# Performance work log

Measured on AMD Instinct MI355X. Metric: run time of the kernel, lower is better.

The kernel has to match this reference:

```python
import jax, jax.numpy as jnp
import numpy as np

B, S, D, H = 1, 3072, 2048, 16
HD = D // H          # head_dim = 128
C = HD // 2          # rotary complex pairs = 64
EPS = 1e-6
WINDOW = 3           # frames of sliding-window attention on each side
L_TOKENS = 256       # tokens per frame (forward arg L)
NUM_FRAMES = S // L_TOKENS


def setup_inputs() -> dict:
    key = jax.random.key(0)
    ks = jax.random.split(key, 5)
    scale = 1.0 / np.sqrt(D)
    x = jax.random.normal(ks[0], (B, S, D), jnp.float32)
    wq = jax.random.normal(ks[1], (D, D), jnp.float32) * scale
    wk = jax.random.normal(ks[2], (D, D), jnp.float32) * scale
    wv = jax.random.normal(ks[3], (D, D), jnp.float32) * scale
    wo = jax.random.normal(ks[4], (D, D), jnp.float32) * scale
    bq = jnp.zeros((D,), jnp.float32)
    bk = jnp.zeros((D,), jnp.float32)
    bv = jnp.zeros((D,), jnp.float32)
    bo = jnp.zeros((D,), jnp.float32)
    gq = jnp.ones((D,), jnp.float32)
    gk = jnp.ones((D,), jnp.float32)
    # rotary freqs as cos/sin of angle t * theta_c (source uses a complex [S,1,C] tensor)
    t = jnp.arange(S, dtype=jnp.float32)
    inv_freq = 1.0 / (10000.0 ** (jnp.arange(C, dtype=jnp.float32) / C))
    ang = t[:, None] * inv_freq[None, :]        # [S, C]
    cos = jnp.cos(ang)[:, None, :]              # [S, 1, C]
    sin = jnp.sin(ang)[:, None, :]              # [S, 1, C]
    return {"x": x, "wq": wq, "bq": bq, "wk": wk, "bk": bk, "wv": wv,
            "bv": bv, "wo": wo, "bo": bo, "gq": gq, "gk": gk,
            "cos": cos, "sin": sin, "f": NUM_FRAMES, "L": L_TOKENS}


def _rms_norm(h, g, eps=EPS):
    # tensor_parallel_rms_norm with tp_size=1: fp32 variance, rsqrt, scale by weight
    hf = h.astype(jnp.float32)
    var = jnp.mean(hf * hf, axis=-1, keepdims=True)
    return (hf * jax.lax.rsqrt(var + eps) * g).astype(h.dtype)


def _rope(h, cos, sin):
    # complex rotation on interleaved (real, imag) pairs per head (rope_apply_for3d)
    b, s, d = h.shape
    hd = 2 * cos.shape[-1]
    n = d // hd
    hr = h.reshape(b, s, n, hd)
    xr, xi = hr[..., 0::2], hr[..., 1::2]       # [b,s,n,C]
    c, sn = cos[None], sin[None]                # [1,s,1,C] broadcast over heads
    yr = xr * c - xi * sn
    yi = xr * sn + xi * c
    y = jnp.stack([yr, yi], axis=-1).reshape(b, s, n, hd)
    return y.reshape(b, s, d)


def reference(x, wq, bq, wk, bk, wv, bv, wo, bo, gq, gk, cos, sin, f, L):
    q = _rope(_rms_norm(x @ wq.T + bq, gq), cos, sin)
    k = _rope(_rms_norm(x @ wk.T + bk, gk), cos, sin)
    v = x @ wv.T + bv
    b, s, d = q.shape
    hd = 2 * cos.shape[-1]
    n = d // hd
    qh = q.reshape(b, s, n, hd)
    kh = k.reshape(b, s, n, hd)
    vh = v.reshape(b, s, n, hd)
    scale = 1.0 / np.sqrt(hd)
    scores = jnp.einsum('bqnd,bknd->bnqk', qh, kh) * scale
    win = L * WINDOW
    idx = jnp.arange(s)
    delta = idx[None, :] - idx[:, None]
    mask = (delta <= win) & (delta >= -win)
    scores = jnp.where(mask[None, None], scores, -jnp.inf)
    probs = jax.nn.softmax(scores, axis=-1)
    out = jnp.einsum('bnqk,bknd->bqnd', probs, vh).reshape(b, s, d)
    return out @ wo.T + bo
```

## Files before the change

kernel.cpp:

```cpp
#include <hip/hip_runtime.h>
#include <stdint.h>

typedef unsigned short u16;
typedef __attribute__((ext_vector_type(8))) short short8;
typedef __attribute__((ext_vector_type(4))) float f32x4;

#define S_LEN 3072
#define D_DIM 2048
#define WIN 768
#define INV_SQRT_HD 0.08838834764831845f
#define M_SHIFT 12.0f

__device__ __forceinline__ u16 f2bf(float x) {
  union { float f; uint32_t u; } v; v.f = x;
  uint32_t r = v.u + 0x7FFFu + ((v.u >> 16) & 1u);
  return (u16)(r >> 16);
}
__device__ __forceinline__ float bf2f(u16 x) {
  union { uint32_t u; float f; } v; v.u = ((uint32_t)x) << 16;
  return v.f;
}

__device__ __forceinline__ void load_lds16(const void* g, void* l) {
  __builtin_amdgcn_global_load_lds(
      (const __attribute__((address_space(1))) void*)g,
      (__attribute__((address_space(3))) void*)l, 16, 0, 0);
}

#define MFMA16(a, b, c) __builtin_amdgcn_mfma_f32_16x16x32_bf16((a), (b), (c), 0, 0, 0)

__global__ __launch_bounds__(256) void k_cvt(const float* __restrict__ in,
                                             u16* __restrict__ out, int n4) {
  int i = blockIdx.x * 256 + threadIdx.x;
  if (i >= n4) return;
  float4 v = ((const float4*)in)[i];
  ushort4 o;
  o.x = f2bf(v.x); o.y = f2bf(v.y); o.z = f2bf(v.z); o.w = f2bf(v.w);
  ((ushort4*)out)[i] = o;
}

__global__ __launch_bounds__(256) void k_cvt_w(const float* __restrict__ w0, const float* __restrict__ w1,
                                               const float* __restrict__ w2, const float* __restrict__ w3,
                                               u16* __restrict__ o0, u16* __restrict__ o1,
                                               u16* __restrict__ o2, u16* __restrict__ o3, int n4each) {
  int i = blockIdx.x * 256 + threadIdx.x;
  int seg = i / n4each, off = i - seg * n4each;
  const float* in = seg == 0 ? w0 : seg == 1 ? w1 : seg == 2 ? w2 : w3;
  u16* out = seg == 0 ? o0 : seg == 1 ? o1 : seg == 2 ? o2 : o3;
  float4 v = ((const float4*)in)[off];
  ushort4 o;
  o.x = f2bf(v.x); o.y = f2bf(v.y); o.z = f2bf(v.z); o.w = f2bf(v.w);
  ((ushort4*)out)[off] = o;
}

__device__ __forceinline__ void gemm_body(const u16* __restrict__ A, const u16* __restrict__ B,
                                          int m0, int n0, int t, f32x4 (*acc)[4],
                                          u16* lA, u16* lB) {
  const int lane = t & 63, w = t >> 6, lo = lane & 15, g = lane >> 4;
  const int wr = w >> 1, wc = w & 1;
  const int srow = t >> 2;
  const int sch = (t & 3) ^ ((srow ^ (srow >> 3)) & 3);
  const u16* ga = A + (size_t)(m0 + srow) * D_DIM + sch * 8;
  const u16* gb = B + (size_t)(n0 + srow) * D_DIM + sch * 8;
  for (int k0 = 0; k0 < D_DIM; k0 += 32) {
    load_lds16(ga + k0, &lA[t * 8]);
    load_lds16(ga + (size_t)64 * D_DIM + k0, &lA[2048 + t * 8]);
    load_lds16(gb + k0, &lB[t * 8]);
    load_lds16(gb + (size_t)64 * D_DIM + k0, &lB[2048 + t * 8]);
    __syncthreads();
    short8 af[4], bfr[4];
#pragma unroll
    for (int m = 0; m < 4; ++m) {
      const int R = wr * 64 + m * 16 + lo;
      af[m] = *(const short8*)&lA[R * 32 + ((g ^ ((R ^ (R >> 3)) & 3)) << 3)];
    }
#pragma unroll
    for (int n = 0; n < 4; ++n) {
      const int R = wc * 64 + n * 16 + lo;
      bfr[n] = *(const short8*)&lB[R * 32 + ((g ^ ((R ^ (R >> 3)) & 3)) << 3)];
    }
#pragma unroll
    for (int m = 0; m < 4; ++m)
#pragma unroll
      for (int n = 0; n < 4; ++n) acc[m][n] = MFMA16(af[m], bfr[n], acc[m][n]);
    __syncthreads();
  }
}

__global__ __launch_bounds__(256) void k_gemm_qkv(const u16* __restrict__ A,
                                                  const u16* __restrict__ Bq, const u16* __restrict__ Bk,
                                                  const u16* __restrict__ Bv,
                                                  const float* __restrict__ bq, const float* __restrict__ bk,
                                                  const float* __restrict__ bv,
                                                  u16* __restrict__ Qb, u16* __restrict__ Kb,
                                                  u16* __restrict__ Vb) {
  __shared__ u16 lA[128 * 32];
  __shared__ u16 lB[128 * 32];
  const int id = blockIdx.x;
  const int xcd = id & 7, local = id >> 3;
  const int m_idx = xcd * 3 + local / 48;
  const int n_idx = local % 48;
  const int m0 = m_idx * 128;
  const int seg = n_idx >> 4, n0 = (n_idx & 15) * 128;
  const u16* B = seg == 0 ? Bq : seg == 1 ? Bk : Bv;
  const float* bias = seg == 0 ? bq : seg == 1 ? bk : bv;
  u16* D = seg == 0 ? Qb : seg == 1 ? Kb : Vb;
  const int t = threadIdx.x;
  const int lane = t & 63, w = t >> 6, lo = lane & 15, g = lane >> 4;
  const int wr = w >> 1, wc = w & 1;
  const f32x4 zero4 = {0.f, 0.f, 0.f, 0.f};
  f32x4 acc[4][4];
#pragma unroll
  for (int m = 0; m < 4; ++m)
#pragma unroll
    for (int n = 0; n < 4; ++n) acc[m][n] = zero4;
  gemm_body(A, B, m0, n0, t, acc, lA, lB);
#pragma unroll
  for (int m = 0; m < 4; ++m) {
    const int row = m0 + wr * 64 + m * 16 + 4 * g;
#pragma unroll
    for (int n = 0; n < 4; ++n) {
      const int col = n0 + wc * 64 + n * 16 + lo;
      const float bb = bias[col];
#pragma unroll
      for (int r = 0; r < 4; ++r)
        D[(size_t)(row + r) * 2048 + col] = f2bf(acc[m][n][r] + bb);
    }
  }
}

__global__ __launch_bounds__(256) void k_gemm_wo(const u16* __restrict__ A,
                                                 const u16* __restrict__ B,
                                                 const float* __restrict__ bias,
                                                 float* __restrict__ C) {
  __shared__ u16 lA[128 * 32];
  __shared__ u16 lB[128 * 32];
  const int id = blockIdx.x;
  const int xcd = id & 7, local = id >> 3;
  const int m_idx = xcd * 3 + local / 16;
  const int n_idx = local % 16;
  const int m0 = m_idx * 128, n0 = n_idx * 128;
  const int t = threadIdx.x;
  const int lane = t & 63, w = t >> 6, lo = lane & 15, g = lane >> 4;
  const int wr = w >> 1, wc = w & 1;
  const f32x4 zero4 = {0.f, 0.f, 0.f, 0.f};
  f32x4 acc[4][4];
#pragma unroll
  for (int m = 0; m < 4; ++m)
#pragma unroll
    for (int n = 0; n < 4; ++n) acc[m][n] = zero4;
  gemm_body(A, B, m0, n0, t, acc, lA, lB);
#pragma unroll
  for (int m = 0; m < 4; ++m) {
    const int row = m0 + wr * 64 + m * 16 + 4 * g;
#pragma unroll
    for (int n = 0; n < 4; ++n) {
      const int col = n0 + wc * 64 + n * 16 + lo;
      const float bb = bias[col];
#pragma unroll
      for (int r = 0; r < 4; ++r)
        C[(size_t)(row + r) * 2048 + col] = acc[m][n][r] + bb;
    }
  }
}

__global__ __launch_bounds__(256) void k_rms_rope_b(const u16* __restrict__ H,
                                                    const float* __restrict__ gain,
                                                    const float* __restrict__ cosT,
                                                    const float* __restrict__ sinT,
                                                    u16* __restrict__ out) {
  const int s = blockIdx.x, t = threadIdx.x;
  const short8 hv = *(const short8*)(H + (size_t)s * D_DIM + t * 8);
  float h[8];
#pragma unroll
  for (int j = 0; j < 8; ++j) h[j] = bf2f((u16)hv[j]);
  float ss = 0.f;
#pragma unroll
  for (int j = 0; j < 8; ++j) ss += h[j] * h[j];
#pragma unroll
  for (int off = 32; off > 0; off >>= 1) ss += __shfl_xor(ss, off);
  __shared__ float red[4];
  if ((t & 63) == 0) red[t >> 6] = ss;
  __syncthreads();
  ss = red[0] + red[1] + red[2] + red[3];
  const float rs = rsqrtf(ss * (1.f / D_DIM) + 1e-6f);
  const float4 g0 = *(const float4*)(gain + t * 8);
  const float4 g1 = *(const float4*)(gain + t * 8 + 4);
  float y[8];
  y[0] = h[0] * rs * g0.x; y[1] = h[1] * rs * g0.y;
  y[2] = h[2] * rs * g0.z; y[3] = h[3] * rs * g0.w;
  y[4] = h[4] * rs * g1.x; y[5] = h[5] * rs * g1.y;
  y[6] = h[6] * rs * g1.z; y[7] = h[7] * rs * g1.w;
  const int cbase = ((t * 8) & 127) >> 1;
  short8 o8;
#pragma unroll
  for (int i = 0; i < 4; ++i) {
    const float cs = cosT[s * 64 + cbase + i];
    const float sn = sinT[s * 64 + cbase + i];
    const float yr = y[2 * i] * cs - y[2 * i + 1] * sn;
    const float yi = y[2 * i] * sn + y[2 * i + 1] * cs;
    o8[2 * i] = (short)f2bf(yr);
    o8[2 * i + 1] = (short)f2bf(yi);
  }
  *(short8*)(out + (size_t)s * D_DIM + t * 8) = o8;
}

__global__ __launch_bounds__(256) void k_transpose(const u16* __restrict__ in,
                                                   u16* __restrict__ out) {
  __shared__ u16 tile[64][72];
  const int s0 = blockIdx.x * 64, d0 = blockIdx.y * 64;
  const int t = threadIdx.x;
  const int r = t >> 3, c8 = (t & 7) * 8;
#pragma unroll
  for (int p = 0; p < 2; ++p) {
    short8 v = *(const short8*)&in[(size_t)(s0 + r + p * 32) * D_DIM + d0 + c8];
#pragma unroll
    for (int j = 0; j < 8; ++j) tile[r + p * 32][c8 + j] = (u16)v[j];
  }
  __syncthreads();
#pragma unroll
  for (int p = 0; p < 2; ++p) {
    const int dr = r + p * 32;
    short8 o;
#pragma unroll
    for (int j = 0; j < 8; ++j) o[j] = (short)tile[c8 + j][dr];
    *(short8*)&out[(size_t)(d0 + dr) * S_LEN + s0 + c8] = o;
  }
}

__global__ __launch_bounds__(256, 3) void k_attn5(const u16* __restrict__ Q,
                                                  const u16* __restrict__ Kmat,
                                                  const u16* __restrict__ Vt,
                                                  u16* __restrict__ Oa,
                                                  u16* __restrict__ Ob,
                                                  float* __restrict__ lbuf) {
  const int qt = blockIdx.x, h = blockIdx.y, z = blockIdx.z;
  const int t = threadIdx.x, w = t >> 6, lane = t & 63, lo = lane & 15, g = lane >> 4;
  const int q0 = qt * 128;
  const int wrow = q0 + w * 32;
  const size_t hoff = (size_t)h * 128;

  __shared__ u16 lK[2][32 * 128];
  __shared__ u16 lV[2][128 * 32];
  __shared__ u16 ldsp[4][32][40];

  short8 qf[2][4];
#pragma unroll
  for (int m = 0; m < 2; ++m) {
    const u16* qp = Q + (size_t)(wrow + m * 16 + lo) * D_DIM + hoff + g * 8;
#pragma unroll
    for (int c = 0; c < 4; ++c) qf[m][c] = *(const short8*)(qp + c * 32);
  }

  const f32x4 zero4 = {0.f, 0.f, 0.f, 0.f};
  f32x4 oacc[2][8];
#pragma unroll
  for (int m = 0; m < 2; ++m)
#pragma unroll
    for (int ct = 0; ct < 8; ++ct) oacc[m][ct] = zero4;
  float lrun[2][4] = {{0.f, 0.f, 0.f, 0.f}, {0.f, 0.f, 0.f, 0.f}};

  int jlo = q0 - WIN; if (jlo < 0) jlo = 0;
  int jhi = q0 + 127 + WIN + 1; if (jhi > S_LEN) jhi = S_LEN;
  const int NT = (jhi - jlo) >> 5;
  const int it0 = z * (NT >> 1), it1 = it0 + (NT >> 1);

  const int krow = t >> 4,          kch  = (t & 15) ^ (krow & 7);
  const int krow1 = (t + 256) >> 4, kch1 = (t & 15) ^ (krow1 & 7);
  const int vrow = t >> 2,          vch  = (t & 3) ^ ((vrow >> 1) & 3);
  const int vrow1 = (t + 256) >> 2, vch1 = (t & 3) ^ ((vrow1 >> 1) & 3);

#define STAGE5(buf, jj)                                                                              \
  do {                                                                                               \
    load_lds16(Kmat + (size_t)((jj) + krow) * D_DIM + hoff + (kch << 3), &lK[buf][t * 8]);           \
    load_lds16(Kmat + (size_t)((jj) + krow1) * D_DIM + hoff + (kch1 << 3), &lK[buf][(t + 256) * 8]); \
    load_lds16(Vt + (size_t)(hoff + vrow) * S_LEN + (jj) + (vch << 3), &lV[buf][t * 8]);             \
    load_lds16(Vt + (size_t)(hoff + vrow1) * S_LEN + (jj) + (vch1 << 3), &lV[buf][(t + 256) * 8]);   \
  } while (0)

  STAGE5(0, jlo + (it0 << 5));
  __syncthreads();
  int cur = 0;
  for (int it = it0; it < it1; ++it) {
    const int j0 = jlo + (it << 5);
    if (it + 1 < it1) STAGE5(cur ^ 1, j0 + 32);

    f32x4 sc[2][2];
    sc[0][0] = zero4; sc[0][1] = zero4; sc[1][0] = zero4; sc[1][1] = zero4;
#pragma unroll
    for (int half = 0; half < 2; ++half) {
#pragma unroll
      for (int c = 0; c < 4; ++c) {
        const short8 kf = *(const short8*)
            &lK[cur][(half * 16 + lo) * 128 + (((g + 4 * c) ^ (lo & 7)) << 3)];
        sc[0][half] = MFMA16(qf[0][c], kf, sc[0][half]);
        sc[1][half] = MFMA16(qf[1][c], kf, sc[1][half]);
      }
    }

    const int dq = j0 - q0;
    const bool interior = (dq >= -640) && (dq <= 736);
#pragma unroll
    for (int m = 0; m < 2; ++m) {
#pragma unroll
      for (int r = 0; r < 4; ++r) {
        float a0 = fmaf(sc[m][0][r], INV_SQRT_HD, -M_SHIFT);
        float a1 = fmaf(sc[m][1][r], INV_SQRT_HD, -M_SHIFT);
        if (!interior) {
          const int dk = j0 + lo - (wrow + m * 16 + 4 * g + r);
          if (dk < -WIN || dk > WIN) a0 = -3e38f;
          if (dk + 16 < -WIN || dk + 16 > WIN) a1 = -3e38f;
        }
        const float p0 = __expf(a0);
        const float p1 = __expf(a1);
        lrun[m][r] += p0 + p1;
        ldsp[w][m * 16 + 4 * g + r][lo] = f2bf(p0);
        ldsp[w][m * 16 + 4 * g + r][16 + lo] = f2bf(p1);
      }
    }

    const short8 pf0 = *(const short8*)&ldsp[w][lo][g * 8];
    const short8 pf1 = *(const short8*)&ldsp[w][16 + lo][g * 8];
#pragma unroll
    for (int ct = 0; ct < 8; ++ct) {
      const short8 vf = *(const short8*)
          &lV[cur][(ct * 16 + lo) * 32 + ((g ^ ((lo >> 1) & 3)) << 3)];
      oacc[0][ct] = MFMA16(pf0, vf, oacc[0][ct]);
      oacc[1][ct] = MFMA16(pf1, vf, oacc[1][ct]);
    }
    __syncthreads();
    cur ^= 1;
  }
#undef STAGE5

#pragma unroll
  for (int off = 8; off > 0; off >>= 1)
#pragma unroll
    for (int m = 0; m < 2; ++m)
#pragma unroll
      for (int r = 0; r < 4; ++r) lrun[m][r] += __shfl_xor(lrun[m][r], off);

  u16* Op = z ? Ob : Oa;
#pragma unroll
  for (int m = 0; m < 2; ++m)
#pragma unroll
    for (int r = 0; r < 4; ++r) {
      const int row = wrow + m * 16 + 4 * g + r;
#pragma unroll
      for (int ct = 0; ct < 8; ++ct)
        Op[(size_t)row * D_DIM + hoff + ct * 16 + lo] = f2bf(oacc[m][ct][r]);
      if (lo == 0) lbuf[(size_t)z * S_LEN * 16 + (size_t)row * 16 + h] = lrun[m][r];
    }
}

__global__ __launch_bounds__(256) void k_combine(const u16* __restrict__ Oa,
                                                 const u16* __restrict__ Ob,
                                                 const float* __restrict__ lbuf,
                                                 u16* __restrict__ out) {
  const int i = blockIdx.x * 256 + threadIdx.x;
  const int s = i >> 8, d8 = (i & 255) * 8, h = d8 >> 7;
  const float la = lbuf[(size_t)s * 16 + h];
  const float lb = lbuf[(size_t)S_LEN * 16 + (size_t)s * 16 + h];
  const float inv = 1.f / (la + lb);
  const size_t base = (size_t)s * D_DIM + d8;
  const short8 a = *(const short8*)(Oa + base);
  const short8 b = *(const short8*)(Ob + base);
  short8 o;
#pragma unroll
  for (int j = 0; j < 8; ++j)
    o[j] = (short)f2bf((bf2f((u16)a[j]) + bf2f((u16)b[j])) * inv);
  *(short8*)(out + base) = o;
}

extern "C" void kernel_launch(void* const* d_in, const int* in_sizes, int n_in,
                              void* d_out, int out_size, void* d_ws, size_t ws_size,
                              hipStream_t stream) {
  const float* x    = (const float*)d_in[0];
  const float* wq   = (const float*)d_in[1];
  const float* bq   = (const float*)d_in[2];
  const float* wk   = (const float*)d_in[3];
  const float* bk   = (const float*)d_in[4];
  const float* wv   = (const float*)d_in[5];
  const float* bv   = (const float*)d_in[6];
  const float* wo   = (const float*)d_in[7];
  const float* bo   = (const float*)d_in[8];
  const float* gq   = (const float*)d_in[9];
  const float* gk   = (const float*)d_in[10];
  const float* cosT = (const float*)d_in[11];
  const float* sinT = (const float*)d_in[12];

  char* ws = (char*)d_ws;
  const size_t WB = (size_t)D_DIM * D_DIM * 2;
  const size_t XB = (size_t)S_LEN * D_DIM * 2;
  u16*   wq_bf = (u16*)(ws);
  u16*   wk_bf = (u16*)(ws + WB);
  u16*   wv_bf = (u16*)(ws + 2 * WB);
  u16*   wo_bf = (u16*)(ws + 3 * WB);
  u16*   x_bf  = (u16*)(ws + 4 * WB);
  u16*   Q0b   = (u16*)(ws + 4 * WB + XB);
  u16*   K0b   = (u16*)(ws + 4 * WB + 2 * XB);
  u16*   V0b   = (u16*)(ws + 4 * WB + 3 * XB);
  float* lbuf  = (float*)(ws + 4 * WB + 4 * XB);
  u16* q_bf = x_bf;
  u16* k_bf = wq_bf;
  u16* vT   = Q0b;
  u16* Ob   = K0b;
  u16* Oa   = (u16*)d_out;
  u16* attn = V0b;

  const int nw4 = (D_DIM * D_DIM) / 4;
  const int nx4 = (S_LEN * D_DIM) / 4;
  k_cvt<<<nx4 / 256, 256, 0, stream>>>(x, x_bf, nx4);
  k_cvt_w<<<4 * nw4 / 256, 256, 0, stream>>>(wq, wk, wv, wo, wq_bf, wk_bf, wv_bf, wo_bf, nw4);

  k_gemm_qkv<<<1152, 256, 0, stream>>>(x_bf, wq_bf, wk_bf, wv_bf, bq, bk, bv, Q0b, K0b, V0b);

  k_rms_rope_b<<<S_LEN, 256, 0, stream>>>(Q0b, gq, cosT, sinT, q_bf);
  k_rms_rope_b<<<S_LEN, 256, 0, stream>>>(K0b, gk, cosT, sinT, k_bf);
  k_transpose<<<dim3(S_LEN / 64, D_DIM / 64), 256, 0, stream>>>(V0b, vT);

  k_attn5<<<dim3(S_LEN / 128, 16, 2), 256, 0, stream>>>(q_bf, k_bf, vT, Oa, Ob, lbuf);
  k_combine<<<(S_LEN * D_DIM / 8) / 256, 256, 0, stream>>>(Oa, Ob, lbuf, attn);

  k_gemm_wo<<<384, 256, 0, stream>>>(attn, wo_bf, bo, (float*)d_out);
}
```

Before: 262.9 us.

## Deepen GEMM K-tile, fuse V transpose into QKV epilogue, merge small kernels

The GEMM main loop now stages 64-wide K slices instead of 32, with an 8-way XOR swizzle. This halves the number of barrier-separated iterations at the cost of twice the LDS per block. The QKV GEMM writes V directly in transposed layout with 4-element vector stores, removing the separate transpose kernel and its extra read/write pass. The x/weight conversion kernels are merged into one launch, and the Q and K RMSNorm+RoPE kernels are merged into one grid, reducing launch count. Workspace aliasing is adjusted so that attn reuses the Q0b buffer.

```diff
diff --git a/kernel.cpp b/kernel.cpp
--- a/kernel.cpp
+++ b/kernel.cpp
@@ -29,60 +29,73 @@
 
 #define MFMA16(a, b, c) __builtin_amdgcn_mfma_f32_16x16x32_bf16((a), (b), (c), 0, 0, 0)
 
-__global__ __launch_bounds__(256) void k_cvt(const float* __restrict__ in,
-                                             u16* __restrict__ out, int n4) {
+__global__ __launch_bounds__(256) void k_cvt_all(const float* __restrict__ x,
+                                                 const float* __restrict__ w0, const float* __restrict__ w1,
+                                                 const float* __restrict__ w2, const float* __restrict__ w3,
+                                                 u16* __restrict__ xo,
+                                                 u16* __restrict__ o0, u16* __restrict__ o1,
+                                                 u16* __restrict__ o2, u16* __restrict__ o3,
+                                                 int n4x, int n4w) {
   int i = blockIdx.x * 256 + threadIdx.x;
-  if (i >= n4) return;
-  float4 v = ((const float4*)in)[i];
-  ushort4 o;
-  o.x = f2bf(v.x); o.y = f2bf(v.y); o.z = f2bf(v.z); o.w = f2bf(v.w);
-  ((ushort4*)out)[i] = o;
-}
-
-__global__ __launch_bounds__(256) void k_cvt_w(const float* __restrict__ w0, const float* __restrict__ w1,
-                                               const float* __restrict__ w2, const float* __restrict__ w3,
-                                               u16* __restrict__ o0, u16* __restrict__ o1,
-                                               u16* __restrict__ o2, u16* __restrict__ o3, int n4each) {
-  int i = blockIdx.x * 256 + threadIdx.x;
-  int seg = i / n4each, off = i - seg * n4each;
-  const float* in = seg == 0 ? w0 : seg == 1 ? w1 : seg == 2 ? w2 : w3;
-  u16* out = seg == 0 ? o0 : seg == 1 ? o1 : seg == 2 ? o2 : o3;
+  const float* in;
+  u16* out;
+  int off;
+  if (i < n4x) {
+    in = x; out = xo; off = i;
+  } else {
+    int j = i - n4x;
+    int seg = j / n4w;
+    off = j - seg * n4w;
+    in = seg == 0 ? w0 : seg == 1 ? w1 : seg == 2 ? w2 : w3;
+    out = seg == 0 ? o0 : seg == 1 ? o1 : seg == 2 ? o2 : o3;
+  }
   float4 v = ((const float4*)in)[off];
   ushort4 o;
   o.x = f2bf(v.x); o.y = f2bf(v.y); o.z = f2bf(v.z); o.w = f2bf(v.w);
   ((ushort4*)out)[off] = o;
 }
 
-__device__ __forceinline__ void gemm_body(const u16* __restrict__ A, const u16* __restrict__ B,
-                                          int m0, int n0, int t, f32x4 (*acc)[4],
-                                          u16* lA, u16* lB) {
+__device__ __forceinline__ void gemm_body64(const u16* __restrict__ A, const u16* __restrict__ B,
+                                            int m0, int n0, int t, f32x4 (*acc)[4],
+                                            u16* lA, u16* lB) {
   const int lane = t & 63, w = t >> 6, lo = lane & 15, g = lane >> 4;
   const int wr = w >> 1, wc = w & 1;
-  const int srow = t >> 2;
-  const int sch = (t & 3) ^ ((srow ^ (srow >> 3)) & 3);
-  const u16* ga = A + (size_t)(m0 + srow) * D_DIM + sch * 8;
-  const u16* gb = B + (size_t)(n0 + srow) * D_DIM + sch * 8;
-  for (int k0 = 0; k0 < D_DIM; k0 += 32) {
-    load_lds16(ga + k0, &lA[t * 8]);
-    load_lds16(ga + (size_t)64 * D_DIM + k0, &lA[2048 + t * 8]);
-    load_lds16(gb + k0, &lB[t * 8]);
-    load_lds16(gb + (size_t)64 * D_DIM + k0, &lB[2048 + t * 8]);
+  const int srow = t >> 3;
+  const int csrc = (t & 7) ^ (srow & 7);
+  const u16* ga = A + (size_t)(m0 + srow) * D_DIM + csrc * 8;
+  const u16* gb = B + (size_t)(n0 + srow) * D_DIM + csrc * 8;
+  for (int k0 = 0; k0 < D_DIM; k0 += 64) {
+    load_lds16(ga + k0,                       &lA[t * 8]);
+    load_lds16(ga + (size_t)32 * D_DIM + k0,  &lA[2048 + t * 8]);
+    load_lds16(ga + (size_t)64 * D_DIM + k0,  &lA[4096 + t * 8]);
+    load_lds16(ga + (size_t)96 * D_DIM + k0,  &lA[6144 + t * 8]);
+    load_lds16(gb + k0,                       &lB[t * 8]);
+    load_lds16(gb + (size_t)32 * D_DIM + k0,  &lB[2048 + t * 8]);
+    load_lds16(gb + (size_t)64 * D_DIM + k0,  &lB[4096 + t * 8]);
+    load_lds16(gb + (size_t)96 * D_DIM + k0,  &lB[6144 + t * 8]);
     __syncthreads();
-    short8 af[4], bfr[4];
+    short8 af[4][2], bfr[4][2];
 #pragma unroll
     for (int m = 0; m < 4; ++m) {
       const int R = wr * 64 + m * 16 + lo;
-      af[m] = *(const short8*)&lA[R * 32 + ((g ^ ((R ^ (R >> 3)) & 3)) << 3)];
+#pragma unroll
+      for (int kk = 0; kk < 2; ++kk)
+        af[m][kk] = *(const short8*)&lA[R * 64 + ((((kk << 2) + g) ^ (R & 7)) << 3)];
     }
 #pragma unroll
     for (int n = 0; n < 4; ++n) {
       const int R = wc * 64 + n * 16 + lo;
-      bfr[n] = *(const short8*)&lB[R * 32 + ((g ^ ((R ^ (R >> 3)) & 3)) << 3)];
+#pragma unroll
+      for (int kk = 0; kk < 2; ++kk)
+        bfr[n][kk] = *(const short8*)&lB[R * 64 + ((((kk << 2) + g) ^ (R & 7)) << 3)];
     }
 #pragma unroll
     for (int m = 0; m < 4; ++m)
 #pragma unroll
-      for (int n = 0; n < 4; ++n) acc[m][n] = MFMA16(af[m], bfr[n], acc[m][n]);
+      for (int n = 0; n < 4; ++n) {
+        acc[m][n] = MFMA16(af[m][0], bfr[n][0], acc[m][n]);
+        acc[m][n] = MFMA16(af[m][1], bfr[n][1], acc[m][n]);
+      }
     __syncthreads();
   }
 }
@@ -93,9 +106,9 @@
                                                   const float* __restrict__ bq, const float* __restrict__ bk,
                                                   const float* __restrict__ bv,
                                                   u16* __restrict__ Qb, u16* __restrict__ Kb,
-                                                  u16* __restrict__ Vb) {
-  __shared__ u16 lA[128 * 32];
-  __shared__ u16 lB[128 * 32];
+                                                  u16* __restrict__ vT) {
+  __shared__ u16 lA[128 * 64];
+  __shared__ u16 lB[128 * 64];
   const int id = blockIdx.x;
   const int xcd = id & 7, local = id >> 3;
   const int m_idx = xcd * 3 + local / 48;
@@ -104,7 +117,6 @@
   const int seg = n_idx >> 4, n0 = (n_idx & 15) * 128;
   const u16* B = seg == 0 ? Bq : seg == 1 ? Bk : Bv;
   const float* bias = seg == 0 ? bq : seg == 1 ? bk : bv;
-  u16* D = seg == 0 ? Qb : seg == 1 ? Kb : Vb;
   const int t = threadIdx.x;
   const int lane = t & 63, w = t >> 6, lo = lane & 15, g = lane >> 4;
   const int wr = w >> 1, wc = w & 1;
@@ -114,17 +126,37 @@
   for (int m = 0; m < 4; ++m)
 #pragma unroll
     for (int n = 0; n < 4; ++n) acc[m][n] = zero4;
-  gemm_body(A, B, m0, n0, t, acc, lA, lB);
-#pragma unroll
-  for (int m = 0; m < 4; ++m) {
-    const int row = m0 + wr * 64 + m * 16 + 4 * g;
-#pragma unroll
-    for (int n = 0; n < 4; ++n) {
-      const int col = n0 + wc * 64 + n * 16 + lo;
-      const float bb = bias[col];
-#pragma unroll
-      for (int r = 0; r < 4; ++r)
-        D[(size_t)(row + r) * 2048 + col] = f2bf(acc[m][n][r] + bb);
+  gemm_body64(A, B, m0, n0, t, acc, lA, lB);
+
+  if (seg == 2) {
+#pragma unroll
+    for (int m = 0; m < 4; ++m) {
+      const int row = m0 + wr * 64 + m * 16 + 4 * g;
+#pragma unroll
+      for (int n = 0; n < 4; ++n) {
+        const int col = n0 + wc * 64 + n * 16 + lo;
+        const float bb = bias[col];
+        ushort4 o;
+        o.x = f2bf(acc[m][n][0] + bb);
+        o.y = f2bf(acc[m][n][1] + bb);
+        o.z = f2bf(acc[m][n][2] + bb);
+        o.w = f2bf(acc[m][n][3] + bb);
+        *(ushort4*)&vT[(size_t)col * S_LEN + row] = o;
+      }
+    }
+  } else {
+    u16* D = seg == 0 ? Qb : Kb;
+#pragma unroll
+    for (int m = 0; m < 4; ++m) {
+      const int row = m0 + wr * 64 + m * 16 + 4 * g;
+#pragma unroll
+      for (int n = 0; n < 4; ++n) {
+        const int col = n0 + wc * 64 + n * 16 + lo;
+        const float bb = bias[col];
+#pragma unroll
+        for (int r = 0; r < 4; ++r)
+          D[(size_t)(row + r) * 2048 + col] = f2bf(acc[m][n][r] + bb);
+      }
     }
   }
 }
@@ -133,8 +165,8 @@
                                                  const u16* __restrict__ B,
                                                  const float* __restrict__ bias,
                                                  float* __restrict__ C) {
-  __shared__ u16 lA[128 * 32];
-  __shared__ u16 lB[128 * 32];
+  __shared__ u16 lA[128 * 64];
+  __shared__ u16 lB[128 * 64];
   const int id = blockIdx.x;
   const int xcd = id & 7, local = id >> 3;
   const int m_idx = xcd * 3 + local / 16;
@@ -149,7 +181,7 @@
   for (int m = 0; m < 4; ++m)
 #pragma unroll
     for (int n = 0; n < 4; ++n) acc[m][n] = zero4;
-  gemm_body(A, B, m0, n0, t, acc, lA, lB);
+  gemm_body64(A, B, m0, n0, t, acc, lA, lB);
 #pragma unroll
   for (int m = 0; m < 4; ++m) {
     const int row = m0 + wr * 64 + m * 16 + 4 * g;
@@ -164,12 +196,14 @@
   }
 }
 
-__global__ __launch_bounds__(256) void k_rms_rope_b(const u16* __restrict__ H,
-                                                    const float* __restrict__ gain,
-                                                    const float* __restrict__ cosT,
-                                                    const float* __restrict__ sinT,
-                                                    u16* __restrict__ out) {
+__global__ __launch_bounds__(256) void k_rms_rope2(const u16* __restrict__ Q0, const u16* __restrict__ K0,
+                                                   const float* __restrict__ gq, const float* __restrict__ gk,
+                                                   const float* __restrict__ cosT, const float* __restrict__ sinT,
+                                                   u16* __restrict__ qo, u16* __restrict__ ko) {
   const int s = blockIdx.x, t = threadIdx.x;
+  const u16* H = blockIdx.y ? K0 : Q0;
+  const float* gain = blockIdx.y ? gk : gq;
+  u16* out = blockIdx.y ? ko : qo;
   const short8 hv = *(const short8*)(H + (size_t)s * D_DIM + t * 8);
   float h[8];
 #pragma unroll
@@ -203,29 +237,6 @@
     o8[2 * i + 1] = (short)f2bf(yi);
   }
   *(short8*)(out + (size_t)s * D_DIM + t * 8) = o8;
-}
-
-__global__ __launch_bounds__(256) void k_transpose(const u16* __restrict__ in,
-                                                   u16* __restrict__ out) {
-  __shared__ u16 tile[64][72];
-  const int s0 = blockIdx.x * 64, d0 = blockIdx.y * 64;
-  const int t = threadIdx.x;
-  const int r = t >> 3, c8 = (t & 7) * 8;
-#pragma unroll
-  for (int p = 0; p < 2; ++p) {
-    short8 v = *(const short8*)&in[(size_t)(s0 + r + p * 32) * D_DIM + d0 + c8];
-#pragma unroll
-    for (int j = 0; j < 8; ++j) tile[r + p * 32][c8 + j] = (u16)v[j];
-  }
-  __syncthreads();
-#pragma unroll
-  for (int p = 0; p < 2; ++p) {
-    const int dr = r + p * 32;
-    short8 o;
-#pragma unroll
-    for (int j = 0; j < 8; ++j) o[j] = (short)tile[c8 + j][dr];
-    *(short8*)&out[(size_t)(d0 + dr) * S_LEN + s0 + c8] = o;
-  }
 }
 
 __global__ __launch_bounds__(256, 3) void k_attn5(const u16* __restrict__ Q,
@@ -399,25 +410,22 @@
   u16*   x_bf  = (u16*)(ws + 4 * WB);
   u16*   Q0b   = (u16*)(ws + 4 * WB + XB);
   u16*   K0b   = (u16*)(ws + 4 * WB + 2 * XB);
-  u16*   V0b   = (u16*)(ws + 4 * WB + 3 * XB);
+  u16*   vT    = (u16*)(ws + 4 * WB + 3 * XB);
   float* lbuf  = (float*)(ws + 4 * WB + 4 * XB);
   u16* q_bf = x_bf;
   u16* k_bf = wq_bf;
-  u16* vT   = Q0b;
   u16* Ob   = K0b;
   u16* Oa   = (u16*)d_out;
-  u16* attn = V0b;
+  u16* attn = Q0b;
 
   const int nw4 = (D_DIM * D_DIM) / 4;
   const int nx4 = (S_LEN * D_DIM) / 4;
-  k_cvt<<<nx4 / 256, 256, 0, stream>>>(x, x_bf, nx4);
-  k_cvt_w<<<4 * nw4 / 256, 256, 0, stream>>>(wq, wk, wv, wo, wq_bf, wk_bf, wv_bf, wo_bf, nw4);
-
-  k_gemm_qkv<<<1152, 256, 0, stream>>>(x_bf, wq_bf, wk_bf, wv_bf, bq, bk, bv, Q0b, K0b, V0b);
-
-  k_rms_rope_b<<<S_LEN, 256, 0, stream>>>(Q0b, gq, cosT, sinT, q_bf);
-  k_rms_rope_b<<<S_LEN, 256, 0, stream>>>(K0b, gk, cosT, sinT, k_bf);
-  k_transpose<<<dim3(S_LEN / 64, D_DIM / 64), 256, 0, stream>>>(V0b, vT);
+  k_cvt_all<<<(nx4 + 4 * nw4) / 256, 256, 0, stream>>>(
+      x, wq, wk, wv, wo, x_bf, wq_bf, wk_bf, wv_bf, wo_bf, nx4, nw4);
+
+  k_gemm_qkv<<<1152, 256, 0, stream>>>(x_bf, wq_bf, wk_bf, wv_bf, bq, bk, bv, Q0b, K0b, vT);
+
+  k_rms_rope2<<<dim3(S_LEN, 2), 256, 0, stream>>>(Q0b, K0b, gq, gk, cosT, sinT, q_bf, k_bf);
 
   k_attn5<<<dim3(S_LEN / 128, 16, 2), 256, 0, stream>>>(q_bf, k_bf, vT, Oa, Ob, lbuf);
   k_combine<<<(S_LEN * D_DIM / 8) / 256, 256, 0, stream>>>(Oa, Ob, lbuf, attn);
```

Result: slower. 301.3 us (+14.6%).
